# Performance work log

Measured on AMD Instinct MI355X. Metric: run time of the kernel, lower is better.

Reference implementation:

```python
import jax, jax.numpy as jnp
import numpy as np

TEMP = 1.0  # softmax temperature from init_kwargs
NEG_BIG = -1e8


def setup_inputs() -> dict:
    key = jax.random.key(0)
    ks = jax.random.split(key, 7)
    T, S, B, H, C, M = 128, 128, 32, 512, 512, 256
    return {
        "hid": jax.random.normal(ks[0], (T, B, H), dtype=jnp.float32),
        "ctx": jax.random.normal(ks[1], (S, B, C), dtype=jnp.float32),
        "ctx_mask": jnp.ones((S, B), dtype=jnp.float32),
        "W_hid2mid": jax.random.normal(ks[2], (M, H), dtype=jnp.float32) * 0.05,
        "W_ctx2mid": jax.random.normal(ks[3], (M, C), dtype=jnp.float32) * 0.05,
        "w_ff": jax.random.normal(ks[4], (M,), dtype=jnp.float32) * 0.05,
        "W_att2hid": jax.random.normal(ks[5], (H, C), dtype=jnp.float32) * 0.05,
    }


def reference(hid, ctx, ctx_mask, W_hid2mid, W_ctx2mid, w_ff, W_att2hid):
    # hid: (T,B,H)  ctx: (S,B,C)  ctx_mask: (S,B)
    hid_m = jnp.einsum('tbh,mh->tbm', hid, W_hid2mid)   # (T,B,M)
    ctx_m = jnp.einsum('sbc,mc->sbm', ctx, W_ctx2mid)   # (S,B,M)
    # broadcast-add -> (S,T,B,M), tanh, project with ff (mid->1), -> scores (S,B,T)
    summed = jnp.tanh(hid_m[None, :, :, :] + ctx_m[:, None, :, :])
    scores = jnp.einsum('stbm,m->sbt', summed, w_ff) / TEMP
    # masked_fill where ctx_mask == 0
    scores = jnp.where(ctx_mask[:, :, None] > 0, scores, NEG_BIG)
    alpha = jax.nn.softmax(scores, axis=0)              # (S,B,T), softmax over S
    attended = jnp.einsum('sbt,sbc->tbc', alpha, ctx)   # (T,B,C)
    z_t = jnp.einsum('tbc,hc->tbh', attended, W_att2hid)  # (T,B,H)
    # torch returns alpha.permute(1,2,0) of (B,T,S) => (T,S,B)
    return (jnp.transpose(alpha, (2, 0, 1)), z_t)
```

## Files before the change

kernel.cpp:

```cpp
#include <hip/hip_runtime.h>
#include <hip/hip_bf16.h>

#define T_DIM 128
#define S_DIM 128
#define B_DIM 32
#define H_DIM 512
#define C_DIM 512
#define M_DIM 256
#define NEG_BIG -1e8f
#define K2LOG2E 2.8853900817779268f

typedef __attribute__((ext_vector_type(8))) short shortx8;
typedef __attribute__((ext_vector_type(4))) float floatx4;

__device__ __forceinline__ unsigned bfpair(float a, float b) {
  unsigned ua = __builtin_bit_cast(unsigned, a); ua += 0x7fffu + ((ua >> 16) & 1u);
  unsigned ub = __builtin_bit_cast(unsigned, b); ub += 0x7fffu + ((ub >> 16) & 1u);
  return (ua >> 16) | (ub & 0xffff0000u);
}
__device__ __forceinline__ uint4 pack2(const float4& a, const float4& b) {
  uint4 o;
  o.x = bfpair(a.x, a.y); o.y = bfpair(a.z, a.w);
  o.z = bfpair(b.x, b.y); o.w = bfpair(b.z, b.w);
  return o;
}
__device__ __forceinline__ ushort bf1(float a) {
  unsigned ua = __builtin_bit_cast(unsigned, a); ua += 0x7fffu + ((ua >> 16) & 1u);
  return (ushort)(ua >> 16);
}
__device__ __forceinline__ float bflo(unsigned u) { return __builtin_bit_cast(float, u << 16); }
__device__ __forceinline__ float bfhi(unsigned u) { return __builtin_bit_cast(float, u & 0xffff0000u); }
__device__ __forceinline__ float4 expand4(unsigned a, unsigned b) {
  return make_float4(bflo(a), bfhi(a), bflo(b), bfhi(b));
}

__global__ __launch_bounds__(256) void gemm_multi(
    const float* __restrict__ hid, const float* __restrict__ Wh, ushort* __restrict__ EHb,
    const float* __restrict__ ctx, const float* __restrict__ Wc, ushort* __restrict__ ECb,
    const float* __restrict__ Wa, ushort* __restrict__ CWT) {
  __shared__ ushort Xs[4096];
  __shared__ ushort Ws[4096];
  const int tid = threadIdx.x;
  const int bid = ((blockIdx.x & 7) << 7) | (blockIdx.x >> 3);

  const float *X, *W;
  int n0, m0;
  if (bid < 512) {
    const int lb = bid & 255;
    n0 = (lb >> 2) << 6; m0 = (lb & 3) << 6;
    X = (bid < 256) ? hid : ctx;
    W = (bid < 256) ? Wh : Wc;
  } else {
    const int lb = bid - 512;
    n0 = (lb >> 3) << 6;
    m0 = (lb & 7) << 6;
    X = ctx;
    W = Wa;
  }

  const int lane = tid & 63, wave = tid >> 6;
  const int wn = wave & 1, wm = wave >> 1;
  const int l15 = lane & 15, lhi = lane >> 4;
  const int r = tid >> 3, c8 = tid & 7;
  const int sw = (c8 ^ (r & 7)) << 4;
  char* xd0 = (char*)Xs + r * 128 + sw;
  char* xd1 = (char*)Xs + (r + 32) * 128 + sw;
  char* wd0 = (char*)Ws + r * 128 + sw;
  char* wd1 = (char*)Ws + (r + 32) * 128 + sw;

  const float* xp0 = X + (size_t)(n0 + r) * 512 + c8 * 8;
  const float* xp1 = X + (size_t)(n0 + r + 32) * 512 + c8 * 8;
  const float* wp0 = W + (size_t)(m0 + r) * 512 + c8 * 8;
  const float* wp1 = W + (size_t)(m0 + r + 32) * 512 + c8 * 8;

  float4 xf0, xf1, xf2, xf3, wf0, wf1, wf2, wf3;
#define LOADXW                                                  \
  xf0 = ((const float4*)xp0)[0]; xf1 = ((const float4*)xp0)[1]; \
  xf2 = ((const float4*)xp1)[0]; xf3 = ((const float4*)xp1)[1]; \
  wf0 = ((const float4*)wp0)[0]; wf1 = ((const float4*)wp0)[1]; \
  wf2 = ((const float4*)wp1)[0]; wf3 = ((const float4*)wp1)[1];
  LOADXW

  floatx4 acc[2][2];
#pragma unroll
  for (int i = 0; i < 2; ++i)
#pragma unroll
    for (int j = 0; j < 2; ++j) acc[i][j] = (floatx4){0.f, 0.f, 0.f, 0.f};

  for (int it = 0; it < 8; ++it) {
    __syncthreads();
    *(uint4*)xd0 = pack2(xf0, xf1);
    *(uint4*)xd1 = pack2(xf2, xf3);
    *(uint4*)wd0 = pack2(wf0, wf1);
    *(uint4*)wd1 = pack2(wf2, wf3);
    __syncthreads();
    if (it < 7) {
      xp0 += 64; xp1 += 64; wp0 += 64; wp1 += 64;
      LOADXW
    }
#pragma unroll
    for (int ks = 0; ks < 2; ++ks) {
      const int slotr = lhi + (ks << 2);
      const int sws = ((slotr ^ (l15 & 7)) << 4);
      shortx8 af[2], bfr[2];
#pragma unroll
      for (int fi = 0; fi < 2; ++fi)
        af[fi] = *(const shortx8*)((const char*)Xs + (wn * 32 + fi * 16 + l15) * 128 + sws);
#pragma unroll
      for (int fj = 0; fj < 2; ++fj)
        bfr[fj] = *(const shortx8*)((const char*)Ws + (wm * 32 + fj * 16 + l15) * 128 + sws);
#pragma unroll
      for (int fi = 0; fi < 2; ++fi)
#pragma unroll
        for (int fj = 0; fj < 2; ++fj)
          acc[fi][fj] = __builtin_amdgcn_mfma_f32_16x16x32_bf16(af[fi], bfr[fj], acc[fi][fj], 0, 0, 0);
    }
  }
#undef LOADXW

  if (bid < 512) {
    ushort* Y = (bid < 256) ? EHb : ECb;
#pragma unroll
    for (int fi = 0; fi < 2; ++fi)
#pragma unroll
      for (int fj = 0; fj < 2; ++fj)
#pragma unroll
        for (int rr = 0; rr < 4; ++rr) {
          const int row = n0 + wn * 32 + fi * 16 + lhi * 4 + rr;
          const int col = m0 + wm * 32 + fj * 16 + l15;
          Y[(size_t)row * M_DIM + col] = bf1(__builtin_amdgcn_exp2f(K2LOG2E * acc[fi][fj][rr]));
        }
  } else {
#pragma unroll
    for (int fi = 0; fi < 2; ++fi)
#pragma unroll
      for (int fj = 0; fj < 2; ++fj)
#pragma unroll
        for (int rr = 0; rr < 4; ++rr) {
          const int row = n0 + wn * 32 + fi * 16 + lhi * 4 + rr;
          const int col = m0 + wm * 32 + fj * 16 + l15;
          CWT[(size_t)row * H_DIM + col] = bf1(acc[fi][fj][rr]);
        }
  }
}

__global__ __launch_bounds__(256) void scores_kernel(
    const ushort* __restrict__ EH, const ushort* __restrict__ EC,
    const float* __restrict__ w_ff, const float* __restrict__ ctx_mask,
    ushort* __restrict__ aws) {
  __shared__ float4 ec[2][8][128];
  __shared__ float4 eh[2][8][8];
  __shared__ float4 wf[2][8];
  __shared__ float msk[S_DIM];
  const int tid = threadIdx.x;
  const int b = blockIdx.y;
  const int t0 = blockIdx.x << 3;
  const int tt = tid >> 6;
  const int st = tid & 63;
  const int sld = tid >> 1, shf = tid & 1;

  if (tid < S_DIM) msk[tid] = ctx_mask[(size_t)tid * B_DIM + b];

  uint4 recu0, recu1;
  uint2 rehu;
  float4 rwf;
#define SLOAD(C)                                                                \
  {                                                                             \
    const ushort* p = EC + ((size_t)sld * B_DIM + b) * M_DIM + ((C) << 5) + (shf << 4); \
    recu0 = ((const uint4*)p)[0];                                               \
    recu1 = ((const uint4*)p)[1];                                               \
    if (tid < 64)                                                               \
      rehu = *(const uint2*)(EH + ((size_t)(t0 + (tid >> 3)) * B_DIM + b) * M_DIM + ((C) << 5) + ((tid & 7) << 2)); \
    if (tid < 8) rwf = *(const float4*)(w_ff + ((C) << 5) + (tid << 2));        \
  }
#define SSTORE(BUF)                                                             \
  {                                                                             \
    const int qb = shf << 2;                                                    \
    ec[BUF][qb + 0][sld] = expand4(recu0.x, recu0.y);                           \
    ec[BUF][qb + 1][sld] = expand4(recu0.z, recu0.w);                           \
    ec[BUF][qb + 2][sld] = expand4(recu1.x, recu1.y);                           \
    ec[BUF][qb + 3][sld] = expand4(recu1.z, recu1.w);                           \
    if (tid < 64) eh[BUF][tid & 7][tid >> 3] = expand4(rehu.x, rehu.y);         \
    if (tid < 8) wf[BUF][tid] = rwf;                                            \
  }

  floatx4 acc[2][2];
#pragma unroll
  for (int i = 0; i < 2; ++i)
#pragma unroll
    for (int j = 0; j < 2; ++j) acc[i][j] = (floatx4){0.f, 0.f, 0.f, 0.f};

  SLOAD(0)
  SSTORE(0)
  __syncthreads();

  for (int c = 0; c < 8; ++c) {
    const int cur = c & 1;
    if (c < 7) SLOAD(c + 1)
#pragma unroll
    for (int q = 0; q < 8; ++q) {
      const float4 w4 = wf[cur][q];
      const float4 e0 = eh[cur][q][2 * tt], e1 = eh[cur][q][2 * tt + 1];
      const float4 c0 = ec[cur][q][st],     c1 = ec[cur][q][st + 64];
#define ACC1(A, E, Cc)                                                 \
  A[0] += w4.x * __builtin_amdgcn_rcpf(E.x * Cc.x + 1.f);              \
  A[1] += w4.y * __builtin_amdgcn_rcpf(E.y * Cc.y + 1.f);              \
  A[2] += w4.z * __builtin_amdgcn_rcpf(E.z * Cc.z + 1.f);              \
  A[3] += w4.w * __builtin_amdgcn_rcpf(E.w * Cc.w + 1.f);
      ACC1(acc[0][0], e0, c0) ACC1(acc[0][1], e0, c1)
      ACC1(acc[1][0], e1, c0) ACC1(acc[1][1], e1, c1)
#undef ACC1
    }
    if (c < 7) {
      SSTORE(cur ^ 1)
      __syncthreads();
    }
  }
#undef SLOAD
#undef SSTORE

  const float mk0 = msk[st], mk1 = msk[st + 64];
  float sc[2][2];
#pragma unroll
  for (int ti = 0; ti < 2; ++ti) {
    const floatx4 a0 = acc[ti][0], a1 = acc[ti][1];
    sc[ti][0] = (mk0 > 0.f) ? -2.f * (a0[0] + a0[1] + a0[2] + a0[3]) : NEG_BIG;
    sc[ti][1] = (mk1 > 0.f) ? -2.f * (a1[0] + a1[1] + a1[2] + a1[3]) : NEG_BIG;
  }
#pragma unroll
  for (int ti = 0; ti < 2; ++ti) {
    float mx = fmaxf(sc[ti][0], sc[ti][1]);
#pragma unroll
    for (int off = 32; off > 0; off >>= 1) mx = fmaxf(mx, __shfl_xor(mx, off));
    const float e0 = __expf(sc[ti][0] - mx), e1 = __expf(sc[ti][1] - mx);
    float sum = e0 + e1;
#pragma unroll
    for (int off = 32; off > 0; off >>= 1) sum += __shfl_xor(sum, off);
    const float rinv = 1.f / sum;
    ushort* w = aws + ((size_t)(t0 + 2 * tt + ti) * B_DIM + b) * S_DIM;
    w[st] = bf1(e0 * rinv);
    w[st + 64] = bf1(e1 * rinv);
  }
}

__global__ __launch_bounds__(256) void epilogue_kernel(
    const ushort* __restrict__ AWS, const ushort* __restrict__ CWT,
    float* __restrict__ z, float* __restrict__ aout) {
  __shared__ char smem[17408];
  const int tid = threadIdx.x;

  if (blockIdx.x >= 512) {
    float (*al)[129] = (float(*)[129])smem;
    const int t = blockIdx.x - 512;
    {
      const int b_ = tid >> 3, q = tid & 7;
      const ushort* src = AWS + ((size_t)t * B_DIM + b_) * S_DIM + q * 16;
      const uint4 u0 = ((const uint4*)src)[0];
      const uint4 u1 = ((const uint4*)src)[1];
      *(float4*)&al[b_][q * 16 + 0]  = expand4(u0.x, u0.y);
      *(float4*)&al[b_][q * 16 + 4]  = expand4(u0.z, u0.w);
      *(float4*)&al[b_][q * 16 + 8]  = expand4(u1.x, u1.y);
      *(float4*)&al[b_][q * 16 + 12] = expand4(u1.z, u1.w);
    }
    __syncthreads();
    {
      const int s = tid >> 1, half = tid & 1;
      float* dst = aout + ((size_t)t * S_DIM + s) * B_DIM + half * 16;
#pragma unroll
      for (int i = 0; i < 4; ++i) {
        float4 o;
        o.x = al[half * 16 + i * 4 + 0][s];
        o.y = al[half * 16 + i * 4 + 1][s];
        o.z = al[half * 16 + i * 4 + 2][s];
        o.w = al[half * 16 + i * 4 + 3][s];
        ((float4*)dst)[i] = o;
      }
    }
    return;
  }

  ushort* Xs = (ushort*)smem;
  ushort* WsT = (ushort*)(smem + 8192);
  const int bid = blockIdx.x;
  const int m0 = (bid & 7) << 6;
  const int n0 = ((bid >> 3) & 1) << 6;
  const int b = bid >> 4;
  const int lane = tid & 63, wave = tid >> 6;
  const int wn = wave & 1, wm = wave >> 1;
  const int l15 = lane & 15, lhi = lane >> 4;
  const int r = tid >> 3, c8 = tid & 7;
  const int lr = tid & 63, ls = tid >> 6;
  const int sw0 = (c8 ^ (r & 7)) << 4;
  char* xr0 = (char*)Xs + r * 128 + sw0;
  char* xr1 = (char*)Xs + (r + 32) * 128 + sw0;

  uint4 xau[2], xbu[2];
  uint4 wv[2][2];
#pragma unroll
  for (int it = 0; it < 2; ++it) {
    xau[it] = *(const uint4*)(AWS + ((size_t)(n0 + r) * B_DIM + b) * S_DIM + it * 64 + c8 * 8);
    xbu[it] = *(const uint4*)(AWS + ((size_t)(n0 + r + 32) * B_DIM + b) * S_DIM + it * 64 + c8 * 8);
    const ushort* q = CWT + ((size_t)(it * 64 + lr) * B_DIM + b) * H_DIM + m0 + ls * 8;
    wv[it][0] = *(const uint4*)q;
    wv[it][1] = *(const uint4*)(q + 32);
  }

  floatx4 acc[2][2];
#pragma unroll
  for (int i = 0; i < 2; ++i)
#pragma unroll
    for (int j = 0; j < 2; ++j) acc[i][j] = (floatx4){0.f, 0.f, 0.f, 0.f};

#pragma unroll
  for (int it = 0; it < 2; ++it) {
    __syncthreads();
    *(uint4*)xr0 = xau[it];
    *(uint4*)xr1 = xbu[it];
#pragma unroll
    for (int q = 0; q < 2; ++q) {
      const int hb = ls * 8 + q * 32;
      const ushort* vs = (const ushort*)&wv[it][q];
#pragma unroll
      for (int i = 0; i < 8; ++i) WsT[(hb + i) * 72 + lr] = vs[i];
    }
    __syncthreads();
#pragma unroll
    for (int ks = 0; ks < 2; ++ks) {
      const int slot = lhi + (ks << 2);
      shortx8 af[2], bfr[2];
#pragma unroll
      for (int fi = 0; fi < 2; ++fi) {
        const int row = wn * 32 + fi * 16 + l15;
        af[fi] = *(const shortx8*)((const char*)Xs + row * 128 + ((slot ^ (row & 7)) << 4));
      }
#pragma unroll
      for (int fj = 0; fj < 2; ++fj) {
        const int col = wm * 32 + fj * 16 + l15;
        bfr[fj] = *(const shortx8*)((const char*)WsT + col * 144 + (slot << 4));
      }
#pragma unroll
      for (int fi = 0; fi < 2; ++fi)
#pragma unroll
        for (int fj = 0; fj < 2; ++fj)
          acc[fi][fj] = __builtin_amdgcn_mfma_f32_16x16x32_bf16(af[fi], bfr[fj], acc[fi][fj], 0, 0, 0);
    }
  }

#pragma unroll
  for (int fi = 0; fi < 2; ++fi)
#pragma unroll
    for (int fj = 0; fj < 2; ++fj)
#pragma unroll
      for (int r2 = 0; r2 < 4; ++r2) {
        const int t = n0 + wn * 32 + fi * 16 + lhi * 4 + r2;
        const int h = m0 + wm * 32 + fj * 16 + l15;
        z[((size_t)t * B_DIM + b) * H_DIM + h] = acc[fi][fj][r2];
      }
}

extern "C" void kernel_launch(void* const* d_in, const int* in_sizes, int n_in,
                              void* d_out, int out_size, void* d_ws, size_t ws_size,
                              hipStream_t stream) {
  const float* hid       = (const float*)d_in[0];
  const float* ctx       = (const float*)d_in[1];
  const float* ctx_mask  = (const float*)d_in[2];
  const float* W_hid2mid = (const float*)d_in[3];
  const float* W_ctx2mid = (const float*)d_in[4];
  const float* w_ff      = (const float*)d_in[5];
  const float* W_att2hid = (const float*)d_in[6];
  float* out = (float*)d_out;
  char*  ws  = (char*)d_ws;

  const size_t MB = 1 << 20;
  ushort* EHb = (ushort*)(ws);
  ushort* ECb = (ushort*)(ws + 2 * MB);
  ushort* AWS = (ushort*)(ws + 4 * MB);
  ushort* CWT = (ushort*)(ws + 5 * MB);
  float* alpha_out = out;
  float* z_out     = out + T_DIM * S_DIM * B_DIM;

  dim3 blk(256);
  gemm_multi<<<1024, blk, 0, stream>>>(hid, W_hid2mid, EHb, ctx, W_ctx2mid, ECb,
                                       W_att2hid, CWT);
  scores_kernel<<<dim3(T_DIM / 8, B_DIM), blk, 0, stream>>>(EHb, ECb, w_ff, ctx_mask, AWS);
  epilogue_kernel<<<640, blk, 0, stream>>>(AWS, CWT, z_out, alpha_out);
}
```

Measured before the change: 49.11 us.

## Move ctx·W_att2hid GEMM into scores kernel to overlap with tanh scoring

Splits the combined GEMM launch so only the EH/EC projections run first. The independent ctx×W_att2hid GEMM (CWT) is interleaved block-by-block with the score/softmax blocks in a new mid kernel sharing one shared-memory buffer. The aim is to shrink the first kernel's critical path and fill the scores kernel's compute with MFMA work from the other GEMM. The cost is a larger shared-memory footprint per block and heterogeneous blocks, which may unbalance scheduling.

After: 192.6 us. 292% more time.

```diff
diff --git a/kernel.cpp b/kernel.cpp
--- a/kernel.cpp
+++ b/kernel.cpp
@@ -34,30 +34,9 @@
   return make_float4(bflo(a), bfhi(a), bflo(b), bfhi(b));
 }
 
-__global__ __launch_bounds__(256) void gemm_multi(
-    const float* __restrict__ hid, const float* __restrict__ Wh, ushort* __restrict__ EHb,
-    const float* __restrict__ ctx, const float* __restrict__ Wc, ushort* __restrict__ ECb,
-    const float* __restrict__ Wa, ushort* __restrict__ CWT) {
-  __shared__ ushort Xs[4096];
-  __shared__ ushort Ws[4096];
-  const int tid = threadIdx.x;
-  const int bid = ((blockIdx.x & 7) << 7) | (blockIdx.x >> 3);
-
-  const float *X, *W;
-  int n0, m0;
-  if (bid < 512) {
-    const int lb = bid & 255;
-    n0 = (lb >> 2) << 6; m0 = (lb & 3) << 6;
-    X = (bid < 256) ? hid : ctx;
-    W = (bid < 256) ? Wh : Wc;
-  } else {
-    const int lb = bid - 512;
-    n0 = (lb >> 3) << 6;
-    m0 = (lb & 7) << 6;
-    X = ctx;
-    W = Wa;
-  }
-
+__device__ __forceinline__ void gemm_core(
+    const float* __restrict__ X, const float* __restrict__ W,
+    int n0, int m0, ushort* Xs, ushort* Ws, int tid, floatx4 acc[2][2]) {
   const int lane = tid & 63, wave = tid >> 6;
   const int wn = wave & 1, wm = wave >> 1;
   const int l15 = lane & 15, lhi = lane >> 4;
@@ -81,12 +60,6 @@
   wf2 = ((const float4*)wp1)[0]; wf3 = ((const float4*)wp1)[1];
   LOADXW
 
-  floatx4 acc[2][2];
-#pragma unroll
-  for (int i = 0; i < 2; ++i)
-#pragma unroll
-    for (int j = 0; j < 2; ++j) acc[i][j] = (floatx4){0.f, 0.f, 0.f, 0.f};
-
   for (int it = 0; it < 8; ++it) {
     __syncthreads();
     *(uint4*)xd0 = pack2(xf0, xf1);
@@ -117,20 +90,67 @@
     }
   }
 #undef LOADXW
-
-  if (bid < 512) {
-    ushort* Y = (bid < 256) ? EHb : ECb;
-#pragma unroll
-    for (int fi = 0; fi < 2; ++fi)
-#pragma unroll
-      for (int fj = 0; fj < 2; ++fj)
-#pragma unroll
-        for (int rr = 0; rr < 4; ++rr) {
-          const int row = n0 + wn * 32 + fi * 16 + lhi * 4 + rr;
-          const int col = m0 + wm * 32 + fj * 16 + l15;
-          Y[(size_t)row * M_DIM + col] = bf1(__builtin_amdgcn_exp2f(K2LOG2E * acc[fi][fj][rr]));
-        }
-  } else {
+}
+
+__global__ __launch_bounds__(256) void gemm_ehec(
+    const float* __restrict__ hid, const float* __restrict__ Wh, ushort* __restrict__ EHb,
+    const float* __restrict__ ctx, const float* __restrict__ Wc, ushort* __restrict__ ECb) {
+  __shared__ ushort Xs[4096];
+  __shared__ ushort Ws[4096];
+  const int tid = threadIdx.x;
+  const int bid = ((blockIdx.x & 7) << 6) | (blockIdx.x >> 3);
+  const int lb = bid & 255;
+  const int n0 = (lb >> 2) << 6, m0 = (lb & 3) << 6;
+  const float* X = (bid < 256) ? hid : ctx;
+  const float* W = (bid < 256) ? Wh : Wc;
+
+  floatx4 acc[2][2];
+#pragma unroll
+  for (int i = 0; i < 2; ++i)
+#pragma unroll
+    for (int j = 0; j < 2; ++j) acc[i][j] = (floatx4){0.f, 0.f, 0.f, 0.f};
+  gemm_core(X, W, n0, m0, Xs, Ws, tid, acc);
+
+  const int lane = tid & 63, wave = tid >> 6;
+  const int wn = wave & 1, wm = wave >> 1;
+  const int l15 = lane & 15, lhi = lane >> 4;
+  ushort* Y = (bid < 256) ? EHb : ECb;
+#pragma unroll
+  for (int fi = 0; fi < 2; ++fi)
+#pragma unroll
+    for (int fj = 0; fj < 2; ++fj)
+#pragma unroll
+      for (int rr = 0; rr < 4; ++rr) {
+        const int row = n0 + wn * 32 + fi * 16 + lhi * 4 + rr;
+        const int col = m0 + wm * 32 + fj * 16 + l15;
+        Y[(size_t)row * M_DIM + col] = bf1(__builtin_amdgcn_exp2f(K2LOG2E * acc[fi][fj][rr]));
+      }
+}
+
+__global__ __launch_bounds__(256, 4) void mid_kernel(
+    const float* __restrict__ ctx, const float* __restrict__ Wa, ushort* __restrict__ CWT,
+    const ushort* __restrict__ EH, const ushort* __restrict__ EC,
+    const float* __restrict__ wff, const float* __restrict__ ctx_mask,
+    ushort* __restrict__ aws) {
+  __shared__ __align__(16) char smem[35584];
+  const int tid = threadIdx.x;
+
+  if ((blockIdx.x & 1) == 0) {
+    const int j = blockIdx.x >> 1;
+    const int n0 = (j >> 3) << 6;
+    const int m0 = (j & 7) << 6;
+    ushort* Xs = (ushort*)smem;
+    ushort* Ws = (ushort*)(smem + 8192);
+    floatx4 acc[2][2];
+#pragma unroll
+    for (int i = 0; i < 2; ++i)
+#pragma unroll
+      for (int jj = 0; jj < 2; ++jj) acc[i][jj] = (floatx4){0.f, 0.f, 0.f, 0.f};
+    gemm_core(ctx, Wa, n0, m0, Xs, Ws, tid, acc);
+
+    const int lane = tid & 63, wave = tid >> 6;
+    const int wn = wave & 1, wm = wave >> 1;
+    const int l15 = lane & 15, lhi = lane >> 4;
 #pragma unroll
     for (int fi = 0; fi < 2; ++fi)
 #pragma unroll
@@ -141,29 +161,26 @@
           const int col = m0 + wm * 32 + fj * 16 + l15;
           CWT[(size_t)row * H_DIM + col] = bf1(acc[fi][fj][rr]);
         }
-  }
-}
-
-__global__ __launch_bounds__(256) void scores_kernel(
-    const ushort* __restrict__ EH, const ushort* __restrict__ EC,
-    const float* __restrict__ w_ff, const float* __restrict__ ctx_mask,
-    ushort* __restrict__ aws) {
-  __shared__ float4 ec[2][8][128];
-  __shared__ float4 eh[2][8][8];
-  __shared__ float4 wf[2][8];
-  __shared__ float msk[S_DIM];
-  const int tid = threadIdx.x;
-  const int b = blockIdx.y;
-  const int t0 = blockIdx.x << 3;
-  const int tt = tid >> 6;
-  const int st = tid & 63;
-  const int sld = tid >> 1, shf = tid & 1;
-
-  if (tid < S_DIM) msk[tid] = ctx_mask[(size_t)tid * B_DIM + b];
-
-  uint4 recu0, recu1;
-  uint2 rehu;
-  float4 rwf;
+    return;
+  }
+
+  {
+    float4 (*ec)[8][128] = (float4 (*)[8][128])(smem);
+    float4 (*eh)[8][8]   = (float4 (*)[8][8])(smem + 32768);
+    float4 (*wf)[8]      = (float4 (*)[8])(smem + 34816);
+    float* msk           = (float*)(smem + 35072);
+    const int j = blockIdx.x >> 1;
+    const int b = j & 31;
+    const int t0 = (j >> 5) << 3;
+    const int tt = tid >> 6;
+    const int st = tid & 63;
+    const int sld = tid >> 1, shf = tid & 1;
+
+    if (tid < S_DIM) msk[tid] = ctx_mask[(size_t)tid * B_DIM + b];
+
+    uint4 recu0, recu1;
+    uint2 rehu;
+    float4 rwf;
 #define SLOAD(C)                                                                \
   {                                                                             \
     const ushort* p = EC + ((size_t)sld * B_DIM + b) * M_DIM + ((C) << 5) + (shf << 4); \
@@ -171,7 +188,7 @@
     recu1 = ((const uint4*)p)[1];                                               \
     if (tid < 64)                                                               \
       rehu = *(const uint2*)(EH + ((size_t)(t0 + (tid >> 3)) * B_DIM + b) * M_DIM + ((C) << 5) + ((tid & 7) << 2)); \
-    if (tid < 8) rwf = *(const float4*)(w_ff + ((C) << 5) + (tid << 2));        \
+    if (tid < 8) rwf = *(const float4*)(wff + ((C) << 5) + (tid << 2));         \
   }
 #define SSTORE(BUF)                                                             \
   {                                                                             \
@@ -184,62 +201,63 @@
     if (tid < 8) wf[BUF][tid] = rwf;                                            \
   }
 
-  floatx4 acc[2][2];
-#pragma unroll
-  for (int i = 0; i < 2; ++i)
-#pragma unroll
-    for (int j = 0; j < 2; ++j) acc[i][j] = (floatx4){0.f, 0.f, 0.f, 0.f};
-
-  SLOAD(0)
-  SSTORE(0)
-  __syncthreads();
-
-  for (int c = 0; c < 8; ++c) {
-    const int cur = c & 1;
-    if (c < 7) SLOAD(c + 1)
-#pragma unroll
-    for (int q = 0; q < 8; ++q) {
-      const float4 w4 = wf[cur][q];
-      const float4 e0 = eh[cur][q][2 * tt], e1 = eh[cur][q][2 * tt + 1];
-      const float4 c0 = ec[cur][q][st],     c1 = ec[cur][q][st + 64];
+    floatx4 acc[2][2];
+#pragma unroll
+    for (int i = 0; i < 2; ++i)
+#pragma unroll
+      for (int jj = 0; jj < 2; ++jj) acc[i][jj] = (floatx4){0.f, 0.f, 0.f, 0.f};
+
+    SLOAD(0)
+    SSTORE(0)
+    __syncthreads();
+
+    for (int c = 0; c < 8; ++c) {
+      const int cur = c & 1;
+      if (c < 7) SLOAD(c + 1)
+#pragma unroll
+      for (int q = 0; q < 8; ++q) {
+        const float4 w4 = wf[cur][q];
+        const float4 e0 = eh[cur][q][2 * tt], e1 = eh[cur][q][2 * tt + 1];
+        const float4 c0 = ec[cur][q][st],     c1 = ec[cur][q][st + 64];
 #define ACC1(A, E, Cc)                                                 \
   A[0] += w4.x * __builtin_amdgcn_rcpf(E.x * Cc.x + 1.f);              \
   A[1] += w4.y * __builtin_amdgcn_rcpf(E.y * Cc.y + 1.f);              \
   A[2] += w4.z * __builtin_amdgcn_rcpf(E.z * Cc.z + 1.f);              \
   A[3] += w4.w * __builtin_amdgcn_rcpf(E.w * Cc.w + 1.f);
-      ACC1(acc[0][0], e0, c0) ACC1(acc[0][1], e0, c1)
-      ACC1(acc[1][0], e1, c0) ACC1(acc[1][1], e1, c1)
+        ACC1(acc[0][0], e0, c0) ACC1(acc[0][1], e0, c1)
+        ACC1(acc[1][0], e1, c0) ACC1(acc[1][1], e1, c1)
 #undef ACC1
-    }
-    if (c < 7) {
-      SSTORE(cur ^ 1)
-      __syncthreads();
-    }
-  }
+      }
+      if (c < 7) {
+        SSTORE(cur ^ 1)
+        __syncthreads();
+      }
+    }
 #undef SLOAD
 #undef SSTORE
 
-  const float mk0 = msk[st], mk1 = msk[st + 64];
-  float sc[2][2];
-#pragma unroll
-  for (int ti = 0; ti < 2; ++ti) {
-    const floatx4 a0 = acc[ti][0], a1 = acc[ti][1];
-    sc[ti][0] = (mk0 > 0.f) ? -2.f * (a0[0] + a0[1] + a0[2] + a0[3]) : NEG_BIG;
-    sc[ti][1] = (mk1 > 0.f) ? -2.f * (a1[0] + a1[1] + a1[2] + a1[3]) : NEG_BIG;
-  }
-#pragma unroll
-  for (int ti = 0; ti < 2; ++ti) {
-    float mx = fmaxf(sc[ti][0], sc[ti][1]);
-#pragma unroll
-    for (int off = 32; off > 0; off >>= 1) mx = fmaxf(mx, __shfl_xor(mx, off));
-    const float e0 = __expf(sc[ti][0] - mx), e1 = __expf(sc[ti][1] - mx);
-    float sum = e0 + e1;
-#pragma unroll
-    for (int off = 32; off > 0; off >>= 1) sum += __shfl_xor(sum, off);
-    const float rinv = 1.f / sum;
-    ushort* w = aws + ((size_t)(t0 + 2 * tt + ti) * B_DIM + b) * S_DIM;
-    w[st] = bf1(e0 * rinv);
-    w[st + 64] = bf1(e1 * rinv);
+    const float mk0 = msk[st], mk1 = msk[st + 64];
+    float sc[2][2];
+#pragma unroll
+    for (int ti = 0; ti < 2; ++ti) {
+      const floatx4 a0 = acc[ti][0], a1 = acc[ti][1];
+      sc[ti][0] = (mk0 > 0.f) ? -2.f * (a0[0] + a0[1] + a0[2] + a0[3]) : NEG_BIG;
+      sc[ti][1] = (mk1 > 0.f) ? -2.f * (a1[0] + a1[1] + a1[2] + a1[3]) : NEG_BIG;
+    }
+#pragma unroll
+    for (int ti = 0; ti < 2; ++ti) {
+      float mx = fmaxf(sc[ti][0], sc[ti][1]);
+#pragma unroll
+      for (int off = 32; off > 0; off >>= 1) mx = fmaxf(mx, __shfl_xor(mx, off));
+      const float e0 = __expf(sc[ti][0] - mx), e1 = __expf(sc[ti][1] - mx);
+      float sum = e0 + e1;
+#pragma unroll
+      for (int off = 32; off > 0; off >>= 1) sum += __shfl_xor(sum, off);
+      const float rinv = 1.f / sum;
+      ushort* w = aws + ((size_t)(t0 + 2 * tt + ti) * B_DIM + b) * S_DIM;
+      w[st] = bf1(e0 * rinv);
+      w[st + 64] = bf1(e1 * rinv);
+    }
   }
 }
 
@@ -380,8 +398,8 @@
   float* z_out     = out + T_DIM * S_DIM * B_DIM;
 
   dim3 blk(256);
-  gemm_multi<<<1024, blk, 0, stream>>>(hid, W_hid2mid, EHb, ctx, W_ctx2mid, ECb,
-                                       W_att2hid, CWT);
-  scores_kernel<<<dim3(T_DIM / 8, B_DIM), blk, 0, stream>>>(EHb, ECb, w_ff, ctx_mask, AWS);
+  gemm_ehec<<<512, blk, 0, stream>>>(hid, W_hid2mid, EHb, ctx, W_ctx2mid, ECb);
+  mid_kernel<<<1024, blk, 0, stream>>>(ctx, W_att2hid, CWT, EHb, ECb,
+                                       w_ff, ctx_mask, AWS);
   epilogue_kernel<<<640, blk, 0, stream>>>(AWS, CWT, z_out, alpha_out);
 }
```
